# Performance work log

Hardware: AMD Instinct MI355X
Metric: run time of the kernel (lower is better)

## Reference

```python
import jax, jax.numpy as jnp
import numpy as np

N, E, D, H = 100000, 1600000, 128, 2
D2 = D * H  # conv2 output dim = out_dim * heads = 256


def setup_inputs() -> dict:
    key = jax.random.key(0)
    ks = jax.random.split(key, 9)
    x = jax.random.normal(ks[0], (N, D), dtype=jnp.float32)
    edge_index = jax.random.randint(ks[1], (2, E), 0, N, dtype=jnp.int64)
    edge_weight = jax.random.uniform(ks[2], (E,), dtype=jnp.float32)
    s = 1.0 / np.sqrt(D)
    W_rel1 = jax.random.normal(ks[3], (D, D), dtype=jnp.float32) * s
    W_root1 = jax.random.normal(ks[4], (D, D), dtype=jnp.float32) * s
    b1 = jnp.zeros((D,), dtype=jnp.float32)
    W_rel2 = jax.random.normal(ks[5], (D, D2), dtype=jnp.float32) * s
    W_root2 = jax.random.normal(ks[6], (D, D2), dtype=jnp.float32) * s
    b2 = jnp.zeros((D2,), dtype=jnp.float32)
    return {"x": x, "edge_index": edge_index, "edge_weight": edge_weight,
            "W_rel1": W_rel1, "b1": b1, "W_root1": W_root1,
            "W_rel2": W_rel2, "b2": b2, "W_root2": W_root2}


def _graph_conv(x, src, dst, edge_weight, W_rel, b, W_root, n_nodes):
    # message: w_e * x_src ; aggregate: mean over incoming edges at dst
    msgs = x[src] * edge_weight[:, None]                       # [E, D]
    summed = jax.ops.segment_sum(msgs, dst, num_segments=n_nodes)  # [N, D]
    cnt = jax.ops.segment_sum(jnp.ones((src.shape[0],), x.dtype), dst,
                              num_segments=n_nodes)
    mean = summed / jnp.maximum(cnt, 1.0)[:, None]
    # GraphConv: lin_rel(aggr) + lin_root(x); bias only on lin_rel
    return mean @ W_rel + b + x @ W_root


def reference(x, edge_index, edge_weight, W_rel1, b1, W_root1, W_rel2, b2, W_root2):
    src, dst = edge_index[0], edge_index[1]
    n = x.shape[0]
    h = _graph_conv(x, src, dst, edge_weight, W_rel1, b1, W_root1, n)
    out = _graph_conv(h, src, dst, edge_weight, W_rel2, b2, W_root2, n)
    return out
```

## Files before the change

kernel.cpp:

```cpp
#include <hip/hip_runtime.h>
#include <hip/hip_bf16.h>

#define D_IN 128
#define SORT_CHUNK 4096
#define NBUCK 256

typedef __attribute__((ext_vector_type(8))) short bf16x8;
typedef __attribute__((ext_vector_type(8))) unsigned short u16x8;
typedef __attribute__((ext_vector_type(4))) float f32x4;


__global__ __launch_bounds__(256) void scan_block_sums(const int* __restrict__ in,
                                                       int* __restrict__ partial,
                                                       int M) {
    __shared__ int sdata[256];
    int b = blockIdx.x, t = threadIdx.x;
    int base = b * 1024 + t * 4;
    int s = 0;
#pragma unroll
    for (int i = 0; i < 4; ++i) {
        int idx = base + i;
        if (idx < M) s += in[idx];
    }
    sdata[t] = s;
    __syncthreads();
    for (int off = 128; off > 0; off >>= 1) {
        if (t < off) sdata[t] += sdata[t + off];
        __syncthreads();
    }
    if (t == 0) partial[b] = sdata[0];
}

__global__ void scan_partials(int* __restrict__ partial, int nb) {
    if (threadIdx.x == 0 && blockIdx.x == 0) {
        int run = 0;
        for (int i = 0; i < nb; ++i) {
            int t = partial[i];
            partial[i] = run;
            run += t;
        }
    }
}

__global__ __launch_bounds__(256) void scan_final(const int* __restrict__ in,
                                                  const int* __restrict__ partial,
                                                  int* __restrict__ outS,
                                                  int M) {
    __shared__ int sdata[256];
    int b = blockIdx.x, t = threadIdx.x;
    int base = b * 1024 + t * 4;
    int v[4];
    int s = 0;
#pragma unroll
    for (int i = 0; i < 4; ++i) {
        int idx = base + i;
        v[i] = (idx < M) ? in[idx] : 0;
        s += v[i];
    }
    sdata[t] = s;
    __syncthreads();
    for (int o = 1; o < 256; o <<= 1) {
        int tmp = 0;
        if (t >= o) tmp = sdata[t - o];
        __syncthreads();
        sdata[t] += tmp;
        __syncthreads();
    }
    int run = partial[b] + (sdata[t] - s);
#pragma unroll
    for (int i = 0; i < 4; ++i) {
        int idx = base + i;
        if (idx < M) outS[idx] = run;
        run += v[i];
    }
}


__global__ __launch_bounds__(256) void bucket_hist_kernel(const int* __restrict__ dst,
                                                          int* __restrict__ bh,
                                                          long long E, int N, int nbe) {
    __shared__ int cnt[NBUCK];
    cnt[threadIdx.x] = 0;
    __syncthreads();
    long long base = (long long)blockIdx.x * SORT_CHUNK;
    long long end = base + SORT_CHUNK;
    if (end > E) end = E;
    for (long long i = base + threadIdx.x; i < end; i += 256) {
        int b = (int)(((long long)dst[i] << 8) / N);
        atomicAdd(&cnt[b], 1);
    }
    __syncthreads();
    bh[threadIdx.x * nbe + blockIdx.x] = cnt[threadIdx.x];
}

__global__ __launch_bounds__(256) void bucket_scatter_kernel(const int* __restrict__ src,
                                                             const int* __restrict__ dst,
                                                             const float* __restrict__ ew,
                                                             const int* __restrict__ S,
                                                             int2* __restrict__ tmp_edges,
                                                             int* __restrict__ tmp_dst,
                                                             long long E, int N, int nbe) {
    __shared__ int base_lds[NBUCK];
    __shared__ int cnt[NBUCK];
    base_lds[threadIdx.x] = S[threadIdx.x * nbe + blockIdx.x];
    cnt[threadIdx.x] = 0;
    __syncthreads();
    long long b0 = (long long)blockIdx.x * SORT_CHUNK;
    long long e1 = b0 + SORT_CHUNK;
    if (e1 > E) e1 = E;
    for (long long i = b0 + threadIdx.x; i < e1; i += 256) {
        int d = dst[i];
        int b = (int)(((long long)d << 8) / N);
        int p = base_lds[b] + atomicAdd(&cnt[b], 1);
        tmp_edges[p] = make_int2(src[i], __float_as_int(ew[i]));
        tmp_dst[p] = d;
    }
}

__global__ __launch_bounds__(256) void bucket_sort_kernel(const int* __restrict__ S,
                                                          const int2* __restrict__ tmp_edges,
                                                          const int* __restrict__ tmp_dst,
                                                          int2* __restrict__ edges,
                                                          int* __restrict__ hist,
                                                          int* __restrict__ off,
                                                          long long E, int N, int nbe) {
    __shared__ int cnt[512];
    __shared__ int tsum[256];
    __shared__ int pos[512];
    const int b = blockIdx.x, t = threadIdx.x;
    const int lo = (int)(((long long)b * N + 255) >> 8);
    const int hi = (int)(((long long)(b + 1) * N + 255) >> 8);
    const int start = S[b * nbe];
    const int end = (b == NBUCK - 1) ? (int)E : S[(b + 1) * nbe];

    cnt[t] = 0;
    cnt[t + 256] = 0;
    __syncthreads();
    for (int i = start + t; i < end; i += 256)
        atomicAdd(&cnt[tmp_dst[i] - lo], 1);
    __syncthreads();

    int a0 = cnt[2 * t], a1 = cnt[2 * t + 1];
    tsum[t] = a0 + a1;
    __syncthreads();
    for (int o = 1; o < 256; o <<= 1) {
        int v = (t >= o) ? tsum[t - o] : 0;
        __syncthreads();
        tsum[t] += v;
        __syncthreads();
    }
    int excl = tsum[t] - (a0 + a1);
    pos[2 * t]     = start + excl;
    pos[2 * t + 1] = start + excl + a0;

    int d0 = lo + 2 * t, d1 = lo + 2 * t + 1;
    if (d0 < hi) { hist[d0] = a0; off[d0] = start + excl + a0; }
    if (d1 < hi) { hist[d1] = a1; off[d1] = start + excl + a0 + a1; }
    __syncthreads();

    for (int i = start + t; i < end; i += 256) {
        int d = tmp_dst[i] - lo;
        int r = atomicAdd(&pos[d], 1);
        edges[r] = tmp_edges[i];
    }
}


__global__ __launch_bounds__(256) void conv_x_kernel(const float* __restrict__ x,
                                                     __hip_bfloat16* __restrict__ xb,
                                                     long long total4) {
    long long i = (long long)blockIdx.x * 256 + threadIdx.x;
    if (i >= total4) return;
    float4 v = reinterpret_cast<const float4*>(x)[i];
    union { ushort4 u; __hip_bfloat162 h2[2]; } o;
    o.h2[0] = __float22bfloat162_rn(make_float2(v.x, v.y));
    o.h2[1] = __float22bfloat162_rn(make_float2(v.z, v.w));
    reinterpret_cast<ushort4*>(xb)[i] = o.u;
}

template <int DOUT>
__global__ __launch_bounds__(256) void conv_w_kernel(const float* __restrict__ Wrel,
                                                     const float* __restrict__ Wroot,
                                                     __hip_bfloat16* __restrict__ Wt) {
    int idx = blockIdx.x * 256 + threadIdx.x;
    if (idx >= DOUT * 256) return;
    int strip  = idx >> 15;
    int within = idx & 32767;
    int s      = within >> 3;
    int j      = within & 7;
    int kchunk = s >> 7;
    int col    = s & 127;
    int k      = kchunk * 8 + j;
    int jcol   = strip * 128 + col;
    float v = (k < 128) ? Wrel[(size_t)k * DOUT + jcol]
                        : Wroot[(size_t)(k - 128) * DOUT + jcol];
    Wt[idx] = __float2bfloat16(v);
}

__global__ __launch_bounds__(256) void aggregate_kernel(const __hip_bfloat16* __restrict__ featb,
                                                        const int2* __restrict__ edges,
                                                        const int* __restrict__ off,
                                                        const int* __restrict__ hist,
                                                        __hip_bfloat16* __restrict__ aggb,
                                                        int N) {
    int node = blockIdx.x * 4 + (threadIdx.x >> 6);
    if (node >= N) return;
    const int lane = threadIdx.x & 63;
    const int g = lane >> 4;
    const int sub = lane & 15;
    const int cnt = hist[node];
    const int end = off[node];
    const int start = end - cnt;
    const float inv = 1.0f / fmaxf((float)cnt, 1.0f);

    const ushort* fb = (const ushort*)featb;
    float acc[8] = {0.f, 0.f, 0.f, 0.f, 0.f, 0.f, 0.f, 0.f};

    int e = start + g;
    for (; e + 4 < end; e += 8) {
        int2 e0 = edges[e];
        int2 e1 = edges[e + 4];
        float w0 = __int_as_float(e0.y);
        float w1 = __int_as_float(e1.y);
        u16x8 r0 = *reinterpret_cast<const u16x8*>(fb + (size_t)e0.x * 128 + sub * 8);
        u16x8 r1 = *reinterpret_cast<const u16x8*>(fb + (size_t)e1.x * 128 + sub * 8);
#pragma unroll
        for (int j = 0; j < 8; ++j) {
            acc[j] += w0 * __int_as_float((unsigned)r0[j] << 16)
                    + w1 * __int_as_float((unsigned)r1[j] << 16);
        }
    }
    if (e < end) {
        int2 e0 = edges[e];
        float w0 = __int_as_float(e0.y);
        u16x8 r0 = *reinterpret_cast<const u16x8*>(fb + (size_t)e0.x * 128 + sub * 8);
#pragma unroll
        for (int j = 0; j < 8; ++j)
            acc[j] += w0 * __int_as_float((unsigned)r0[j] << 16);
    }

#pragma unroll
    for (int j = 0; j < 8; ++j) {
        acc[j] += __shfl_xor(acc[j], 16, 64);
        acc[j] += __shfl_xor(acc[j], 32, 64);
    }

    if (g == 0) {
        union { u16x8 u; __hip_bfloat162 h2[4]; } o;
#pragma unroll
        for (int j = 0; j < 4; ++j)
            o.h2[j] = __float22bfloat162_rn(make_float2(acc[2 * j] * inv, acc[2 * j + 1] * inv));
        *reinterpret_cast<u16x8*>((ushort*)aggb + (size_t)node * 128 + sub * 8) = o.u;
    }
}

template <int DOUT, bool OUT_BF16>
__global__ __launch_bounds__(512, 4) void gemm_mfma5(const __hip_bfloat16* __restrict__ Arel,
                                                     const __hip_bfloat16* __restrict__ Aroot,
                                                     const __hip_bfloat16* __restrict__ Wt,
                                                     const float* __restrict__ bias,
                                                     void* __restrict__ outp,
                                                     int M) {
    constexpr int NY = DOUT / 128;
    __shared__ __align__(16) unsigned char Bs[65536];

    const int nb = gridDim.x;
    const int orig = blockIdx.x;
    const int xcd = orig & 7;
    const int lid = orig >> 3;
    const int q = nb >> 3, r = nb & 7;
    const int wgid = (xcd < r ? xcd * (q + 1) : r * (q + 1) + (xcd - r) * q) + lid;

    const int ty = wgid % NY;
    const int tx = wgid / NY;
    const int tid = threadIdx.x;
    const int lane = tid & 63;
    const int wave = tid >> 6;
    const int lr = lane & 15;
    const int lk = lane >> 4;

    const char* wbase = (const char*)Wt + (size_t)ty * 65536;
#pragma unroll
    for (int i = 0; i < 8; ++i) {
        int s = i * 512 + tid;
        __builtin_amdgcn_global_load_lds(
            (const __attribute__((address_space(1))) unsigned int*)(wbase + (size_t)s * 16),
            (__attribute__((address_space(3))) unsigned int*)(&Bs[s * 16]),
            16, 0, 0);
    }

    const int wr = wave >> 2;
    const int wc = wave & 3;
    const int mbase = tx * 128 + wr * 64;
    const int nloc = wc * 32;
    const int nbase = ty * 128 + nloc;

    const short* arow[4];
    const short* xrow[4];
#pragma unroll
    for (int mi = 0; mi < 4; ++mi) {
        int row = mbase + mi * 16 + lr;
        int rc = row < M ? row : M - 1;
        arow[mi] = (const short*)Arel  + (size_t)rc * 128 + lk * 8;
        xrow[mi] = (const short*)Aroot + (size_t)rc * 128 + lk * 8;
    }

    __syncthreads();

    f32x4 zero = {0.f, 0.f, 0.f, 0.f};
    f32x4 acc[4][2];
#pragma unroll
    for (int mi = 0; mi < 4; ++mi)
#pragma unroll
        for (int ni = 0; ni < 2; ++ni) acc[mi][ni] = zero;

#pragma unroll
    for (int kk = 0; kk < 8; ++kk) {
        bf16x8 a[4], b[2];
#pragma unroll
        for (int mi = 0; mi < 4; ++mi)
            a[mi] = (kk < 4)
                ? *reinterpret_cast<const bf16x8*>(arow[mi] + kk * 32)
                : *reinterpret_cast<const bf16x8*>(xrow[mi] + (kk - 4) * 32);
#pragma unroll
        for (int ni = 0; ni < 2; ++ni) {
            int slot = (kk * 4 + lk) * 128 + nloc + ni * 16 + lr;
            b[ni] = *reinterpret_cast<const bf16x8*>(&Bs[slot * 16]);
        }
#pragma unroll
        for (int mi = 0; mi < 4; ++mi)
#pragma unroll
            for (int ni = 0; ni < 2; ++ni)
                acc[mi][ni] = __builtin_amdgcn_mfma_f32_16x16x32_bf16(a[mi], b[ni], acc[mi][ni], 0, 0, 0);
    }

#pragma unroll
    for (int mi = 0; mi < 4; ++mi)
#pragma unroll
        for (int ni = 0; ni < 2; ++ni) {
            int col = nbase + ni * 16 + lr;
            float bv = bias[col];
#pragma unroll
            for (int rr = 0; rr < 4; ++rr) {
                int row = mbase + mi * 16 + lk * 4 + rr;
                if (row < M) {
                    float v = acc[mi][ni][rr] + bv;
                    if (OUT_BF16)
                        ((__hip_bfloat16*)outp)[(size_t)row * DOUT + col] = __float2bfloat16(v);
                    else
                        __builtin_nontemporal_store(v, (float*)outp + (size_t)row * DOUT + col);
                }
            }
        }
}


extern "C" void kernel_launch(void* const* d_in, const int* in_sizes, int n_in,
                              void* d_out, int out_size, void* d_ws, size_t ws_size,
                              hipStream_t stream) {
    const float* x      = (const float*)d_in[0];
    const int*   ei     = (const int*)d_in[1];
    const float* ew     = (const float*)d_in[2];
    const float* Wrel1  = (const float*)d_in[3];
    const float* b1     = (const float*)d_in[4];
    const float* Wroot1 = (const float*)d_in[5];
    const float* Wrel2  = (const float*)d_in[6];
    const float* b2     = (const float*)d_in[7];
    const float* Wroot2 = (const float*)d_in[8];
    float* out = (float*)d_out;

    const int N = in_sizes[0] / D_IN;
    const long long E = in_sizes[2];
    const int* src = ei;
    const int* dst = ei + E;

    const int nbe = (int)((E + SORT_CHUNK - 1) / SORT_CHUNK);
    const int M = nbe * NBUCK;
    const int nbM = (M + 1023) / 1024;

    int* hist = (int*)d_ws;
    int* off  = hist + N;
    int* part = off + N;
    int2* edges = (int2*)(part + 128);
    __hip_bfloat16* agg1b = (__hip_bfloat16*)(edges + E);
    __hip_bfloat16* xb    = agg1b + (size_t)N * D_IN;
    __hip_bfloat16* agg2b = xb    + (size_t)N * D_IN;
    __hip_bfloat16* hb    = agg2b + (size_t)N * D_IN;
    __hip_bfloat16* Wt1   = hb    + (size_t)N * D_IN;
    __hip_bfloat16* Wt2   = Wt1   + 128 * 256;

    int* bh      = (int*)agg1b;
    int* S       = bh + M;
    int* tmp_dst = S + M;
    int2* tmp_edges = (int2*)agg2b;

    bucket_hist_kernel<<<nbe, 256, 0, stream>>>(dst, bh, E, N, nbe);
    scan_block_sums<<<nbM, 256, 0, stream>>>(bh, part, M);
    scan_partials<<<1, 64, 0, stream>>>(part, nbM);
    scan_final<<<nbM, 256, 0, stream>>>(bh, part, S, M);
    bucket_scatter_kernel<<<nbe, 256, 0, stream>>>(src, dst, ew, S, tmp_edges, tmp_dst, E, N, nbe);
    bucket_sort_kernel<<<NBUCK, 256, 0, stream>>>(S, tmp_edges, tmp_dst, edges, hist, off, E, N, nbe);

    {
        long long total4 = (long long)N * D_IN / 4;
        conv_x_kernel<<<(int)((total4 + 255) / 256), 256, 0, stream>>>(x, xb, total4);
        conv_w_kernel<128><<<(128 * 256 + 255) / 256, 256, 0, stream>>>(Wrel1, Wroot1, Wt1);
        conv_w_kernel<256><<<(256 * 256 + 255) / 256, 256, 0, stream>>>(Wrel2, Wroot2, Wt2);
    }

    const int ab = (N + 3) / 4;
    const int gx = (N + 127) / 128;

    aggregate_kernel<<<ab, 256, 0, stream>>>(xb, edges, off, hist, agg1b, N);
    gemm_mfma5<128, true><<<gx * 1, 512, 0, stream>>>(agg1b, xb, Wt1, b1, hb, N);

    aggregate_kernel<<<ab, 256, 0, stream>>>(hb, edges, off, hist, agg2b, N);
    gemm_mfma5<256, false><<<gx * 2, 512, 0, stream>>>(agg2b, hb, Wt2, b2, out, N);
}
```

Before: 327.3 us.

## Shrink GEMM tile to 64x64 and stage A operand in LDS via direct loads

The GEMM now uses 64x64 output tiles with 256-thread blocks instead of 128x128 tiles with 512 threads. Both the A operands (aggregated and root features) and the weight strip are loaded into LDS with global_load_lds, instead of each wave reading A rows straight from global memory. The weight pre-layout kernel is changed to 64-column strips to match. Smaller tiles give more blocks and less LDS per block, at the cost of loading A rows again for every column strip.

```diff
diff --git a/kernel.cpp b/kernel.cpp
--- a/kernel.cpp
+++ b/kernel.cpp
@@ -184,14 +184,14 @@
                                                      __hip_bfloat16* __restrict__ Wt) {
     int idx = blockIdx.x * 256 + threadIdx.x;
     if (idx >= DOUT * 256) return;
-    int strip  = idx >> 15;
-    int within = idx & 32767;
+    int strip  = idx >> 14;
+    int within = idx & 16383;
     int s      = within >> 3;
     int j      = within & 7;
-    int kchunk = s >> 7;
-    int col    = s & 127;
+    int kchunk = s >> 6;
+    int col    = s & 63;
     int k      = kchunk * 8 + j;
-    int jcol   = strip * 128 + col;
+    int jcol   = strip * 64 + col;
     float v = (k < 128) ? Wrel[(size_t)k * DOUT + jcol]
                         : Wroot[(size_t)(k - 128) * DOUT + jcol];
     Wt[idx] = __float2bfloat16(v);
@@ -255,14 +255,15 @@
 }
 
 template <int DOUT, bool OUT_BF16>
-__global__ __launch_bounds__(512, 4) void gemm_mfma5(const __hip_bfloat16* __restrict__ Arel,
+__global__ __launch_bounds__(256, 2) void gemm_mfma6(const __hip_bfloat16* __restrict__ Arel,
                                                      const __hip_bfloat16* __restrict__ Aroot,
                                                      const __hip_bfloat16* __restrict__ Wt,
                                                      const float* __restrict__ bias,
                                                      void* __restrict__ outp,
                                                      int M) {
-    constexpr int NY = DOUT / 128;
-    __shared__ __align__(16) unsigned char Bs[65536];
+    constexpr int NY = DOUT / 64;
+    __shared__ __align__(16) unsigned char As[32768];
+    __shared__ __align__(16) unsigned char Bs[32768];
 
     const int nb = gridDim.x;
     const int orig = blockIdx.x;
@@ -279,70 +280,67 @@
     const int lr = lane & 15;
     const int lk = lane >> 4;
 
-    const char* wbase = (const char*)Wt + (size_t)ty * 65536;
+    const char* wbase = (const char*)Wt + (size_t)ty * 32768;
 #pragma unroll
     for (int i = 0; i < 8; ++i) {
-        int s = i * 512 + tid;
+        int s = i * 256 + tid;
         __builtin_amdgcn_global_load_lds(
             (const __attribute__((address_space(1))) unsigned int*)(wbase + (size_t)s * 16),
             (__attribute__((address_space(3))) unsigned int*)(&Bs[s * 16]),
             16, 0, 0);
     }
-
-    const int wr = wave >> 2;
-    const int wc = wave & 3;
-    const int mbase = tx * 128 + wr * 64;
+#pragma unroll
+    for (int i = 0; i < 8; ++i) {
+        int s = i * 256 + tid;
+        int kc = s >> 6;
+        int rloc = s & 63;
+        int row = tx * 64 + rloc;
+        int rc = row < M ? row : M - 1;
+        const short* srcp = (i < 4)
+            ? (const short*)Arel  + (size_t)rc * 128 + kc * 8
+            : (const short*)Aroot + (size_t)rc * 128 + (kc - 16) * 8;
+        __builtin_amdgcn_global_load_lds(
+            (const __attribute__((address_space(1))) unsigned int*)srcp,
+            (__attribute__((address_space(3))) unsigned int*)(&As[s * 16]),
+            16, 0, 0);
+    }
+
+    const int wr = wave >> 1;
+    const int wc = wave & 1;
+    const int mloc = wr * 32;
     const int nloc = wc * 32;
-    const int nbase = ty * 128 + nloc;
-
-    const short* arow[4];
-    const short* xrow[4];
-#pragma unroll
-    for (int mi = 0; mi < 4; ++mi) {
-        int row = mbase + mi * 16 + lr;
-        int rc = row < M ? row : M - 1;
-        arow[mi] = (const short*)Arel  + (size_t)rc * 128 + lk * 8;
-        xrow[mi] = (const short*)Aroot + (size_t)rc * 128 + lk * 8;
-    }
 
     __syncthreads();
 
     f32x4 zero = {0.f, 0.f, 0.f, 0.f};
-    f32x4 acc[4][2];
-#pragma unroll
-    for (int mi = 0; mi < 4; ++mi)
-#pragma unroll
-        for (int ni = 0; ni < 2; ++ni) acc[mi][ni] = zero;
+    f32x4 acc[2][2] = {{zero, zero}, {zero, zero}};
 
 #pragma unroll
     for (int kk = 0; kk < 8; ++kk) {
-        bf16x8 a[4], b[2];
-#pragma unroll
-        for (int mi = 0; mi < 4; ++mi)
-            a[mi] = (kk < 4)
-                ? *reinterpret_cast<const bf16x8*>(arow[mi] + kk * 32)
-                : *reinterpret_cast<const bf16x8*>(xrow[mi] + (kk - 4) * 32);
-#pragma unroll
-        for (int ni = 0; ni < 2; ++ni) {
-            int slot = (kk * 4 + lk) * 128 + nloc + ni * 16 + lr;
-            b[ni] = *reinterpret_cast<const bf16x8*>(&Bs[slot * 16]);
-        }
-#pragma unroll
-        for (int mi = 0; mi < 4; ++mi)
+        const int chunk = kk * 4 + lk;
+        bf16x8 a[2], b[2];
+#pragma unroll
+        for (int mi = 0; mi < 2; ++mi)
+            a[mi] = *reinterpret_cast<const bf16x8*>(&As[(chunk * 64 + mloc + mi * 16 + lr) * 16]);
+#pragma unroll
+        for (int ni = 0; ni < 2; ++ni)
+            b[ni] = *reinterpret_cast<const bf16x8*>(&Bs[(chunk * 64 + nloc + ni * 16 + lr) * 16]);
+#pragma unroll
+        for (int mi = 0; mi < 2; ++mi)
 #pragma unroll
             for (int ni = 0; ni < 2; ++ni)
                 acc[mi][ni] = __builtin_amdgcn_mfma_f32_16x16x32_bf16(a[mi], b[ni], acc[mi][ni], 0, 0, 0);
     }
 
 #pragma unroll
-    for (int mi = 0; mi < 4; ++mi)
+    for (int mi = 0; mi < 2; ++mi)
 #pragma unroll
         for (int ni = 0; ni < 2; ++ni) {
-            int col = nbase + ni * 16 + lr;
+            int col = ty * 64 + nloc + ni * 16 + lr;
             float bv = bias[col];
 #pragma unroll
             for (int rr = 0; rr < 4; ++rr) {
-                int row = mbase + mi * 16 + lk * 4 + rr;
+                int row = tx * 64 + mloc + mi * 16 + lk * 4 + rr;
                 if (row < M) {
                     float v = acc[mi][ni][rr] + bv;
                     if (OUT_BF16)
@@ -409,11 +407,11 @@
     }
 
     const int ab = (N + 3) / 4;
-    const int gx = (N + 127) / 128;
+    const int gx64 = (N + 63) / 64;
 
     aggregate_kernel<<<ab, 256, 0, stream>>>(xb, edges, off, hist, agg1b, N);
-    gemm_mfma5<128, true><<<gx * 1, 512, 0, stream>>>(agg1b, xb, Wt1, b1, hb, N);
+    gemm_mfma6<128, true><<<gx64 * 2, 256, 0, stream>>>(agg1b, xb, Wt1, b1, hb, N);
 
     aggregate_kernel<<<ab, 256, 0, stream>>>(hb, edges, off, hist, agg2b, N);
-    gemm_mfma5<256, false><<<gx * 2, 512, 0, stream>>>(agg2b, hb, Wt2, b2, out, N);
-}
+    gemm_mfma6<256, false><<<gx64 * 4, 256, 0, stream>>>(agg2b, hb, Wt2, b2, out, N);
+}
```

Measured after the change: 308.7 us. 5.7% less time.

## Make GEMM persistent with per-wave 16-row panels over full 128-column strip

Applied to the files above, without the earlier changes.

Replaces the one-block-per-128-row-tile GEMM with a persistent grid of 512 blocks. Each block loads its weight strip into LDS once, and each wave then loops over 16-row panels covering all 128 output columns. This amortizes the 64KB weight staging across many row panels instead of reloading it per tile, and changes per-wave tiling from 64x32 to 16x128. The final fp32 output store also switches from nontemporal to a regular store. Risks include more LDS reads per MFMA and less A-operand reuse, plus grid-size choices that may not balance well across CUs.

```diff
diff --git a/kernel.cpp b/kernel.cpp
--- a/kernel.cpp
+++ b/kernel.cpp
@@ -188,9 +188,9 @@
     int within = idx & 32767;
     int s      = within >> 3;
     int j      = within & 7;
-    int kchunk = s >> 7;
+    int kc     = s >> 7;
     int col    = s & 127;
-    int k      = kchunk * 8 + j;
+    int k      = kc * 8 + j;
     int jcol   = strip * 128 + col;
     float v = (k < 128) ? Wrel[(size_t)k * DOUT + jcol]
                         : Wroot[(size_t)(k - 128) * DOUT + jcol];
@@ -255,29 +255,25 @@
 }
 
 template <int DOUT, bool OUT_BF16>
-__global__ __launch_bounds__(512, 4) void gemm_mfma5(const __hip_bfloat16* __restrict__ Arel,
+__global__ __launch_bounds__(512, 4) void gemm_mfma8(const __hip_bfloat16* __restrict__ Arel,
                                                      const __hip_bfloat16* __restrict__ Aroot,
                                                      const __hip_bfloat16* __restrict__ Wt,
                                                      const float* __restrict__ bias,
                                                      void* __restrict__ outp,
-                                                     int M) {
+                                                     int M, int blocks_per_strip) {
     constexpr int NY = DOUT / 128;
     __shared__ __align__(16) unsigned char Bs[65536];
 
     const int nb = gridDim.x;
     const int orig = blockIdx.x;
     const int xcd = orig & 7;
-    const int lid = orig >> 3;
+    const int lid0 = orig >> 3;
     const int q = nb >> 3, r = nb & 7;
-    const int wgid = (xcd < r ? xcd * (q + 1) : r * (q + 1) + (xcd - r) * q) + lid;
-
+    const int wgid = (xcd < r ? xcd * (q + 1) : r * (q + 1) + (xcd - r) * q) + lid0;
     const int ty = wgid % NY;
-    const int tx = wgid / NY;
+    const int blk = wgid / NY;
+
     const int tid = threadIdx.x;
-    const int lane = tid & 63;
-    const int wave = tid >> 6;
-    const int lr = lane & 15;
-    const int lk = lane >> 4;
 
     const char* wbase = (const char*)Wt + (size_t)ty * 65536;
 #pragma unroll
@@ -288,70 +284,62 @@
             (__attribute__((address_space(3))) unsigned int*)(&Bs[s * 16]),
             16, 0, 0);
     }
-
-    const int wr = wave >> 2;
-    const int wc = wave & 3;
-    const int mbase = tx * 128 + wr * 64;
-    const int nloc = wc * 32;
-    const int nbase = ty * 128 + nloc;
-
-    const short* arow[4];
-    const short* xrow[4];
-#pragma unroll
-    for (int mi = 0; mi < 4; ++mi) {
-        int row = mbase + mi * 16 + lr;
+    __syncthreads();
+
+    const int lane = tid & 63;
+    const int wave = tid >> 6;
+    const int lr = lane & 15;
+    const int lk = lane >> 4;
+    const int nwtot = blocks_per_strip * 8;
+    const int gw = blk * 8 + wave;
+    const int npan = (M + 15) >> 4;
+
+    f32x4 zero = {0.f, 0.f, 0.f, 0.f};
+
+    for (int p = gw; p < npan; p += nwtot) {
+        int row = p * 16 + lr;
         int rc = row < M ? row : M - 1;
-        arow[mi] = (const short*)Arel  + (size_t)rc * 128 + lk * 8;
-        xrow[mi] = (const short*)Aroot + (size_t)rc * 128 + lk * 8;
-    }
-
-    __syncthreads();
-
-    f32x4 zero = {0.f, 0.f, 0.f, 0.f};
-    f32x4 acc[4][2];
-#pragma unroll
-    for (int mi = 0; mi < 4; ++mi)
-#pragma unroll
-        for (int ni = 0; ni < 2; ++ni) acc[mi][ni] = zero;
-
-#pragma unroll
-    for (int kk = 0; kk < 8; ++kk) {
-        bf16x8 a[4], b[2];
-#pragma unroll
-        for (int mi = 0; mi < 4; ++mi)
-            a[mi] = (kk < 4)
-                ? *reinterpret_cast<const bf16x8*>(arow[mi] + kk * 32)
-                : *reinterpret_cast<const bf16x8*>(xrow[mi] + (kk - 4) * 32);
-#pragma unroll
-        for (int ni = 0; ni < 2; ++ni) {
-            int slot = (kk * 4 + lk) * 128 + nloc + ni * 16 + lr;
-            b[ni] = *reinterpret_cast<const bf16x8*>(&Bs[slot * 16]);
+        const short* ar = (const short*)Arel  + (size_t)rc * 128 + lk * 8;
+        const short* xr = (const short*)Aroot + (size_t)rc * 128 + lk * 8;
+
+        bf16x8 a[8];
+#pragma unroll
+        for (int kk = 0; kk < 4; ++kk) {
+            a[kk]     = *reinterpret_cast<const bf16x8*>(ar + kk * 32);
+            a[4 + kk] = *reinterpret_cast<const bf16x8*>(xr + kk * 32);
         }
-#pragma unroll
-        for (int mi = 0; mi < 4; ++mi)
-#pragma unroll
-            for (int ni = 0; ni < 2; ++ni)
-                acc[mi][ni] = __builtin_amdgcn_mfma_f32_16x16x32_bf16(a[mi], b[ni], acc[mi][ni], 0, 0, 0);
-    }
-
-#pragma unroll
-    for (int mi = 0; mi < 4; ++mi)
-#pragma unroll
-        for (int ni = 0; ni < 2; ++ni) {
-            int col = nbase + ni * 16 + lr;
+
+        f32x4 acc[8];
+#pragma unroll
+        for (int ni = 0; ni < 8; ++ni) acc[ni] = zero;
+
+#pragma unroll
+        for (int kk = 0; kk < 8; ++kk) {
+            const int chunk = kk * 4 + lk;
+#pragma unroll
+            for (int ni = 0; ni < 8; ++ni) {
+                bf16x8 b = *reinterpret_cast<const bf16x8*>(&Bs[(chunk * 128 + ni * 16 + lr) * 16]);
+                acc[ni] = __builtin_amdgcn_mfma_f32_16x16x32_bf16(a[kk], b, acc[ni], 0, 0, 0);
+            }
+        }
+
+#pragma unroll
+        for (int ni = 0; ni < 8; ++ni) {
+            int col = ty * 128 + ni * 16 + lr;
             float bv = bias[col];
 #pragma unroll
             for (int rr = 0; rr < 4; ++rr) {
-                int row = mbase + mi * 16 + lk * 4 + rr;
-                if (row < M) {
-                    float v = acc[mi][ni][rr] + bv;
+                int rw = p * 16 + lk * 4 + rr;
+                if (rw < M) {
+                    float v = acc[ni][rr] + bv;
                     if (OUT_BF16)
-                        ((__hip_bfloat16*)outp)[(size_t)row * DOUT + col] = __float2bfloat16(v);
+                        ((__hip_bfloat16*)outp)[(size_t)rw * DOUT + col] = __float2bfloat16(v);
                     else
-                        __builtin_nontemporal_store(v, (float*)outp + (size_t)row * DOUT + col);
+                        ((float*)outp)[(size_t)rw * DOUT + col] = v;
                 }
             }
         }
+    }
 }
 
 
@@ -409,11 +397,10 @@
     }
 
     const int ab = (N + 3) / 4;
-    const int gx = (N + 127) / 128;
 
     aggregate_kernel<<<ab, 256, 0, stream>>>(xb, edges, off, hist, agg1b, N);
-    gemm_mfma5<128, true><<<gx * 1, 512, 0, stream>>>(agg1b, xb, Wt1, b1, hb, N);
+    gemm_mfma8<128, true><<<512, 512, 0, stream>>>(agg1b, xb, Wt1, b1, hb, N, 512);
 
     aggregate_kernel<<<ab, 256, 0, stream>>>(hb, edges, off, hist, agg2b, N);
-    gemm_mfma5<256, false><<<gx * 2, 512, 0, stream>>>(agg2b, hb, Wt2, b2, out, N);
-}
+    gemm_mfma8<256, false><<<512, 512, 0, stream>>>(agg2b, hb, Wt2, b2, out, N, 256);
+}
```

Result: slower. 576.6 us (+76.2%).
